# Kernel optimization log

Measured on AMD Instinct MI355X. Metric: run time of the kernel, lower is better.

The kernel has to match this reference:

```python
import jax, jax.numpy as jnp
import numpy as np

N = 50000      # nodes
E = 800000     # edges
D = 200        # in_dim = hid_dim
R = 230        # num_rels
B = 100        # bdd bases -> submat = D // B = 2
S = D // B     # submatrix size (2)


def setup_inputs() -> dict:
    key = jax.random.key(0)
    ks = jax.random.split(key, 16)
    node_feat = jax.random.normal(ks[0], (N, D), dtype=jnp.float32)
    dynamic_emb = jax.random.normal(ks[1], (N, 1, D), dtype=jnp.float32)
    src = jax.random.randint(ks[2], (E,), 0, N, dtype=jnp.int32)
    dst = jax.random.randint(ks[3], (E,), 0, N, dtype=jnp.int32)
    etypes = jax.random.randint(ks[4], (E,), 0, R, dtype=jnp.int32)
    # BDD relational weights per layer: [R, B, S, S]
    w1 = jax.random.normal(ks[5], (R, B, S, S), dtype=jnp.float32) * 0.1
    loop_w1 = jax.random.normal(ks[6], (D, D), dtype=jnp.float32) * 0.05
    b1 = jnp.zeros((D,), dtype=jnp.float32)
    w2 = jax.random.normal(ks[7], (R, B, S, S), dtype=jnp.float32) * 0.1
    loop_w2 = jax.random.normal(ks[8], (D, D), dtype=jnp.float32) * 0.05
    b2 = jnp.zeros((D,), dtype=jnp.float32)
    # single-layer vanilla RNN (tanh) params
    W_ih = jax.random.normal(ks[9], (D, D), dtype=jnp.float32) * 0.05
    W_hh = jax.random.normal(ks[10], (D, D), dtype=jnp.float32) * 0.05
    b_ih = jnp.zeros((D,), dtype=jnp.float32)
    b_hh = jnp.zeros((D,), dtype=jnp.float32)
    return {"node_feat": node_feat, "dynamic_emb": dynamic_emb,
            "src": src, "dst": dst, "etypes": etypes,
            "w1": w1, "loop_w1": loop_w1, "b1": b1,
            "w2": w2, "loop_w2": loop_w2, "b2": b2,
            "W_ih": W_ih, "W_hh": W_hh, "b_ih": b_ih, "b_hh": b_hh}


def _rel_graph_conv_bdd(x, src, dst, etypes, edge_norm, w, loop_w, b):
    # gather source feats and apply per-edge-type block-diagonal transform
    xs = x[src].reshape(E, B, S)                     # [E, B, S]
    msg = jnp.einsum('ebi,ebio->ebo', xs, w[etypes]) # [E, B, S]
    msg = msg.reshape(E, D) * edge_norm              # edge-norm scaling
    agg = jax.ops.segment_sum(msg, dst, num_segments=N)  # scatter-add to dst
    return agg + x @ loop_w + b                      # self-loop + bias


def reference(node_feat, dynamic_emb, src, dst, etypes,
              w1, loop_w1, b1, w2, loop_w2, b2,
              W_ih, W_hh, b_ih, b_hh):
    # edge_norm = dst node norm = 1 / in-degree
    deg = jax.ops.segment_sum(jnp.ones((E,), jnp.float32), dst, num_segments=N)
    node_norm = jnp.where(deg > 0, 1.0 / jnp.maximum(deg, 1.0), 0.0)
    edge_norm = node_norm[dst][:, None]              # [E, 1]

    # RGCN layer 1 (tanh activation), layer 2 (no activation); dropout=eval
    h = _rel_graph_conv_bdd(node_feat, src, dst, etypes, edge_norm, w1, loop_w1, b1)
    h = jnp.tanh(h)
    h = _rel_graph_conv_bdd(h, src, dst, etypes, edge_norm, w2, loop_w2, b2)

    # single-step vanilla RNN: hn = tanh(x W_ih^T + b_ih + h0 W_hh^T + b_hh)
    h0 = dynamic_emb[:, 0, :]                        # [N, D]
    hn = jnp.tanh(h @ W_ih.T + b_ih + h0 @ W_hh.T + b_hh)
    return hn[:, None, :]                            # [N, 1, D]
```

## Files before the change

kernel.cpp:

```cpp
#include <hip/hip_runtime.h>

#define N_NODES 50000
#define N_EDGES 800000
#define DIM     200
#define NBLK    100
#define NRELS   230
#define NB_SCAN 196
#define KPAD    224
#define KPN     256
#define NROWPAD 50048
#define NFRAG8  (8 * 14 * 64)

typedef __attribute__((ext_vector_type(8)))  short short8;
typedef __attribute__((ext_vector_type(16))) float f32x16;

__device__ __forceinline__ unsigned short f2bf(float f) {
    unsigned u = __float_as_uint(f);
    u += 0x7fffu + ((u >> 16) & 1u);
    return (unsigned short)(u >> 16);
}

__device__ __forceinline__ float bflo(unsigned u) { return __uint_as_float(u << 16); }
__device__ __forceinline__ float bfhi(unsigned u) { return __uint_as_float(u & 0xffff0000u); }
__device__ __forceinline__ float b2f(unsigned short u) { return __uint_as_float((unsigned)u << 16); }

__device__ __forceinline__ float tanh_fast(float x) {
    float xa = fminf(fmaxf(x, -15.0f), 15.0f);
    float e = __expf(2.0f * xa);
    return (e - 1.0f) / (e + 1.0f);
}

__device__ __forceinline__ int uread(int v, int l) {
    return __builtin_amdgcn_readlane(v, l);
}

#if __has_builtin(__builtin_amdgcn_fdot2_f32_bf16)
typedef __bf16 bf16x2 __attribute__((ext_vector_type(2)));
__device__ __forceinline__ float dot2bf(unsigned a, unsigned b, float c) {
    return __builtin_amdgcn_fdot2_f32_bf16(
        __builtin_bit_cast(bf16x2, a), __builtin_bit_cast(bf16x2, b), c, false);
}
#define CMP(XU, WU, M0, M1, M2, M3)                                     \
    { M0 = dot2bf(XU.x, WU.x, M0); M1 = dot2bf(XU.x, WU.y, M1);         \
      M2 = dot2bf(XU.y, WU.z, M2); M3 = dot2bf(XU.y, WU.w, M3); }
#else
#define CMP(XU, WU, M0, M1, M2, M3)                                     \
    { float x0 = bflo(XU.x), x1 = bfhi(XU.x);                           \
      float x2 = bflo(XU.y), x3 = bfhi(XU.y);                           \
      M0 += x0 * bflo(WU.x) + x1 * bfhi(WU.x);                          \
      M1 += x0 * bflo(WU.y) + x1 * bfhi(WU.y);                          \
      M2 += x2 * bflo(WU.z) + x3 * bfhi(WU.z);                          \
      M3 += x2 * bflo(WU.w) + x3 * bfhi(WU.w); }
#endif

#define SWZ5(rr, off) ((unsigned)((rr) * 512 + (off)) ^ ((unsigned)((rr) & 15) << 4))

__global__ void deg_int_kernel(const int* __restrict__ dst, int* __restrict__ degi) {
    int e = blockIdx.x * blockDim.x + threadIdx.x;
    if (e < N_EDGES) atomicAdd(&degi[dst[e]], 1);
}

__global__ __launch_bounds__(256) void scanA(const int* __restrict__ degi,
                                             int* __restrict__ pos,
                                             int* __restrict__ bsum) {
    __shared__ int tmp[256];
    int t = threadIdx.x;
    int g = blockIdx.x * 256 + t;
    int v = (g < N_NODES) ? degi[g] : 0;
    tmp[t] = v;
    __syncthreads();
    for (int off = 1; off < 256; off <<= 1) {
        int xv = (t >= off) ? tmp[t - off] : 0;
        __syncthreads();
        tmp[t] += xv;
        __syncthreads();
    }
    if (g < N_NODES) pos[g] = tmp[t] - v;
    if (t == 255) bsum[blockIdx.x] = tmp[255];
}

__global__ __launch_bounds__(256) void scanC2(int* __restrict__ pos, const int* __restrict__ bsum) {
    __shared__ int tmp[256];
    __shared__ int excl[256];
    int t = threadIdx.x;
    int v = (t < NB_SCAN) ? bsum[t] : 0;
    tmp[t] = v;
    __syncthreads();
    for (int off = 1; off < 256; off <<= 1) {
        int xv = (t >= off) ? tmp[t - off] : 0;
        __syncthreads();
        tmp[t] += xv;
        __syncthreads();
    }
    excl[t] = tmp[t] - v;
    __syncthreads();
    int add = excl[blockIdx.x];
    int g = blockIdx.x * 256 + t;
    if (g < N_NODES) pos[g] += add;
}

__global__ void fill_kernel(const int* __restrict__ src, const int* __restrict__ dst,
                            const int* __restrict__ et,
                            int* __restrict__ pos, int* __restrict__ se) {
    int e = blockIdx.x * blockDim.x + threadIdx.x;
    if (e < N_EDGES) {
        int d = dst[e];
        int slot = atomicAdd(&pos[d], 1);
        se[slot] = src[e] | (et[e] << 16);
    }
}

__global__ void prep_feat(const float* __restrict__ x, const float* __restrict__ de,
                          unsigned short* __restrict__ hb, unsigned short* __restrict__ h0b) {
    const int HALF = NROWPAD * (KPAD / 2);
    int idx = blockIdx.x * blockDim.x + threadIdx.x;
    if (idx >= 2 * HALF) return;
    const float* src = (idx < HALF) ? x : de;
    unsigned short* dstp = (idx < HALF) ? hb : h0b;
    int j = (idx < HALF) ? idx : idx - HALF;
    int row = j / (KPAD / 2), cu = j % (KPAD / 2);
    unsigned pk = 0;
    if (row < N_NODES && cu < 100) {
        float2 v = *(const float2*)(src + (size_t)row * DIM + cu * 2);
        pk = (unsigned)f2bf(v.x) | ((unsigned)f2bf(v.y) << 16);
    }
    *(unsigned*)(dstp + (size_t)j * 2) = pk;
}

__global__ void prep_wbs(const float* __restrict__ w1, const float* __restrict__ w2,
                         unsigned short* __restrict__ w1b, unsigned short* __restrict__ w2b) {
    const int HALF = NRELS * NBLK;
    int idx = blockIdx.x * blockDim.x + threadIdx.x;
    if (idx >= 2 * HALF) return;
    const float* w = (idx < HALF) ? w1 : w2;
    unsigned short* o = (idx < HALF) ? w1b : w2b;
    int j = (idx < HALF) ? idx : idx - HALF;
    float4 v = *(const float4*)(w + (size_t)j * 4);
    unsigned c0 = (unsigned)f2bf(v.x) | ((unsigned)f2bf(v.z) << 16);
    unsigned c1 = (unsigned)f2bf(v.y) | ((unsigned)f2bf(v.w) << 16);
    *(uint2*)(o + (size_t)j * 4) = make_uint2(c0, c1);
}

__global__ void prep_frags(const float* __restrict__ lw1, const float* __restrict__ wih,
                           const float* __restrict__ whh,
                           unsigned short* __restrict__ w1f, unsigned short* __restrict__ wihf,
                           unsigned short* __restrict__ whhf) {
    int idx = blockIdx.x * blockDim.x + threadIdx.x;
    if (idx >= 3 * NFRAG8) return;
    int sec = idx / NFRAG8, f = idx % NFRAG8;
    const float* w = (sec == 0) ? lw1 : (sec == 1) ? wih : whh;
    unsigned short* o = (sec == 0) ? w1f : (sec == 1) ? wihf : whhf;
    int l = f & 63;
    int ks = (f >> 6) % 14;
    int nt = f / (14 * 64);
    int n  = nt * 32 + (l & 31);
    int k0 = ks * 16 + (l >> 5) * 8;
    unsigned short v[8];
    #pragma unroll
    for (int j = 0; j < 8; ++j) {
        int k = k0 + j;
        float val = 0.0f;
        if (n < DIM && k < DIM)
            val = (sec == 0) ? w[k * DIM + n] : w[n * DIM + k];
        v[j] = f2bf(val);
    }
    *(uint4*)(o + (size_t)f * 8) = *(uint4*)v;
}

__global__ __launch_bounds__(256) void mcompute(
        const float* __restrict__ w2, const float* __restrict__ wih,
        const float* __restrict__ b2, const float* __restrict__ b_ih,
        const float* __restrict__ b_hh, float* __restrict__ Mt) {
    int idx = blockIdx.x * blockDim.x + threadIdx.x;
    if (idx >= (DIM + 1) * DIM) return;
    int k = idx / DIM, n = idx % DIM;
    const float* ar = (k < DIM) ? (w2 + (size_t)k * DIM) : b2;
    const float* br = wih + (size_t)n * DIM;
    float s0 = 0.f, s1 = 0.f, s2 = 0.f, s3 = 0.f;
    #pragma unroll 5
    for (int q = 0; q < DIM; q += 4) {
        float4 a = *(const float4*)(ar + q);
        float4 b = *(const float4*)(br + q);
        s0 += a.x * b.x; s1 += a.y * b.y; s2 += a.z * b.z; s3 += a.w * b.w;
    }
    float s = (s0 + s1) + (s2 + s3);
    if (k == DIM) s += b_ih[n] + b_hh[n];
    Mt[idx] = s;
}

__global__ void prep_Mf2(const float* __restrict__ Mt, unsigned short* __restrict__ Mf,
                         float* __restrict__ biasv) {
    int idx = blockIdx.x * blockDim.x + threadIdx.x;
    if (idx < NFRAG8) {
        int l = idx & 63;
        int ks = (idx >> 6) % 14;
        int nt = idx / (14 * 64);
        int n  = nt * 32 + (l & 31);
        int k0 = ks * 16 + (l >> 5) * 8;
        unsigned short v[8];
        #pragma unroll
        for (int j = 0; j < 8; ++j) {
            int k = k0 + j;
            v[j] = f2bf((n < DIM && k < DIM) ? Mt[k * DIM + n] : 0.0f);
        }
        *(uint4*)(Mf + (size_t)idx * 8) = *(uint4*)v;
    } else if (idx < NFRAG8 + KPN) {
        int n = idx - NFRAG8;
        biasv[n] = (n < DIM) ? Mt[DIM * DIM + n] : 0.0f;
    }
}

#define GL(QQ, XU, WU)                                                  \
    { int p_ = uread(sv, (QQ)); int s_ = p_ & 0xffff; int r_ = p_ >> 16;\
      XU = *(const uint2*)(x  + (size_t)s_ * KPAD + xoff);              \
      WU = *(const uint4*)(wb + (size_t)r_ * (NBLK * 4) + woff); }

__global__ __launch_bounds__(256) void gatherB(
        const unsigned short* __restrict__ x,
        const int*   __restrict__ se,
        const int*   __restrict__ endpos,
        const int*   __restrict__ degi,
        const unsigned short* __restrict__ wb,
        unsigned short* __restrict__ agg) {
    int node = (blockIdx.x * blockDim.x + threadIdx.x) >> 6;
    int lane = threadIdx.x & 63;
    if (node >= N_NODES) return;
    int deg = __builtin_amdgcn_readfirstlane(degi[node]);
    const bool act = (lane < 50);
    int cl   = act ? lane : 49;
    int xoff = 4 * cl;
    int woff = 8 * cl;

    if (deg == 0) {
        if (lane < 56) *(uint2*)(agg + (size_t)node * KPAD + 4 * lane) = make_uint2(0u, 0u);
        return;
    }
    int end   = __builtin_amdgcn_readfirstlane(endpos[node]);
    int start = end - deg;

    float m0A = 0.f, m1A = 0.f, m2A = 0.f, m3A = 0.f;
    float m0B = 0.f, m1B = 0.f, m2B = 0.f, m3B = 0.f;

    for (int base = start; base < end; base += 64) {
        int cnt = end - base; if (cnt > 64) cnt = 64;
        int sv = se[base + (lane < cnt ? lane : cnt - 1)];

        uint2 X0 = {0,0}, X1 = {0,0}, X2 = {0,0}, X3 = {0,0};
        uint4 W0 = {0,0,0,0}, W1 = {0,0,0,0}, W2 = {0,0,0,0}, W3 = {0,0,0,0};

        GL(0, X0, W0);
        if (cnt > 1) GL(1, X1, W1);
        if (cnt > 2) GL(2, X2, W2);

        for (int q = 0; q < cnt; q += 4) {
            if (q + 3 < cnt) GL(q + 3, X3, W3);
            CMP(X0, W0, m0A, m1A, m2A, m3A);
            if (q + 4 < cnt) GL(q + 4, X0, W0);
            if (q + 1 < cnt) CMP(X1, W1, m0B, m1B, m2B, m3B);
            if (q + 5 < cnt) GL(q + 5, X1, W1);
            if (q + 2 < cnt) CMP(X2, W2, m0A, m1A, m2A, m3A);
            if (q + 6 < cnt) GL(q + 6, X2, W2);
            if (q + 3 < cnt) CMP(X3, W3, m0B, m1B, m2B, m3B);
        }
    }
    float nrm = 1.0f / (float)deg;
    uint2 ov = make_uint2(0u, 0u);
    if (act) {
        ov.x = (unsigned)f2bf((m0A + m0B) * nrm) | ((unsigned)f2bf((m1A + m1B) * nrm) << 16);
        ov.y = (unsigned)f2bf((m2A + m2B) * nrm) | ((unsigned)f2bf((m3A + m3B) * nrm) << 16);
    }
    if (lane < 56) *(uint2*)(agg + (size_t)node * KPAD + 4 * lane) = ov;
}

__global__ __launch_bounds__(256) void gemm1_kernel(
        unsigned short* xb_hb,
        const unsigned short* __restrict__ agg1,
        const float* __restrict__ b1,
        const unsigned short* __restrict__ w1f) {
    __shared__ __align__(16) unsigned short s_a[32 * KPN];
    int row0 = blockIdx.x * 32;
    int tid = threadIdx.x;
    for (int i = tid; i < 32 * 32; i += 256) {
        int rr = i >> 5, ch = i & 31;
        uint4 v = {0, 0, 0, 0};
        if (ch < 28) v = *(const uint4*)(xb_hb + (size_t)(row0 + rr) * KPAD + ch * 8);
        *(uint4*)((char*)s_a + SWZ5(rr, ch * 16)) = v;
    }
    __syncthreads();

    int l = tid & 63, wv = tid >> 6;
    int rl = l & 31, hl = l >> 5;
    int ntlo = wv * 2;
    const unsigned short* wb = w1f + (size_t)(ntlo * 14) * 512 + l * 8;

    f32x16 acc0 = {}, acc1 = {};
    short8 aC  = *(const short8*)((const char*)s_a + SWZ5(rl, (hl * 8) * 2));
    short8 b0C = *(const short8*)(wb);
    short8 b1C = *(const short8*)(wb + 14 * 512);
    #pragma unroll
    for (int ks = 0; ks < 13; ++ks) {
        short8 aN = {}, b0N = {}, b1N = {};
        if (ks < 12) {
            aN  = *(const short8*)((const char*)s_a + SWZ5(rl, ((ks + 1) * 16 + hl * 8) * 2));
            b0N = *(const short8*)(wb + (ks + 1) * 512);
            b1N = *(const short8*)(wb + 14 * 512 + (ks + 1) * 512);
        }
        acc0 = __builtin_amdgcn_mfma_f32_32x32x16_bf16(aC, b0C, acc0, 0, 0, 0);
        acc1 = __builtin_amdgcn_mfma_f32_32x32x16_bf16(aC, b1C, acc1, 0, 0, 0);
        aC = aN; b0C = b0N; b1C = b1N;
    }
    __syncthreads();

    #pragma unroll
    for (int t = 0; t < 2; ++t) {
        f32x16 ac = t ? acc1 : acc0;
        int gc = (ntlo + t) * 32 + rl;
        if (gc >= KPAD) continue;
        float bias = (gc < DIM) ? b1[gc] : 0.0f;
        #pragma unroll
        for (int r = 0; r < 16; ++r) {
            int gr = row0 + (r & 3) + 8 * (r >> 2) + 4 * hl;
            float v = 0.0f;
            if (gc < DIM && gr < N_NODES)
                v = ac[r] + b2f(agg1[(size_t)gr * KPAD + gc]) + bias;
            xb_hb[(size_t)gr * KPAD + gc] = f2bf(tanh_fast(v));
        }
    }
}

__global__ __launch_bounds__(256) void gemm2_kernel(
        const unsigned short* __restrict__ hb,
        const unsigned short* __restrict__ aggp,
        const unsigned short* __restrict__ h0b,
        const unsigned short* __restrict__ Mf,
        const unsigned short* __restrict__ wihf,
        const unsigned short* __restrict__ whhf,
        const float* __restrict__ biasv,
        float* __restrict__ out) {
    __shared__ __align__(16) unsigned short s_h[32 * KPN];
    __shared__ __align__(16) unsigned short s_g[32 * KPN];
    __shared__ __align__(16) unsigned short s_e[32 * KPN];
    int row0 = blockIdx.x * 32;
    int tid = threadIdx.x;
    for (int i = tid; i < 32 * 32; i += 256) {
        int rr = i >> 5, ch = i & 31;
        uint4 vh = {0,0,0,0}, vg = {0,0,0,0}, ve = {0,0,0,0};
        if (ch < 28) {
            size_t off = (size_t)(row0 + rr) * KPAD + ch * 8;
            vh = *(const uint4*)(hb   + off);
            vg = *(const uint4*)(aggp + off);
            ve = *(const uint4*)(h0b  + off);
        }
        unsigned sw = SWZ5(rr, ch * 16);
        *(uint4*)((char*)s_h + sw) = vh;
        *(uint4*)((char*)s_g + sw) = vg;
        *(uint4*)((char*)s_e + sw) = ve;
    }
    __syncthreads();

    int l = tid & 63, wv = tid >> 6;
    int rl = l & 31, hl = l >> 5;
    int ntlo = wv * 2;
    const unsigned short* pm = Mf   + (size_t)(ntlo * 14) * 512 + l * 8;
    const unsigned short* pi = wihf + (size_t)(ntlo * 14) * 512 + l * 8;
    const unsigned short* ph = whhf + (size_t)(ntlo * 14) * 512 + l * 8;

    f32x16 a0 = {}, a1 = {};
    unsigned off0 = SWZ5(rl, (hl * 8) * 2);
    short8 hC  = *(const short8*)((const char*)s_h + off0);
    short8 gC  = *(const short8*)((const char*)s_g + off0);
    short8 eC  = *(const short8*)((const char*)s_e + off0);
    short8 m0C = *(const short8*)(pm);
    short8 m1C = *(const short8*)(pm + 14 * 512);
    short8 i0C = *(const short8*)(pi);
    short8 i1C = *(const short8*)(pi + 14 * 512);
    short8 h0C = *(const short8*)(ph);
    short8 h1C = *(const short8*)(ph + 14 * 512);
    #pragma unroll
    for (int ks = 0; ks < 13; ++ks) {
        short8 hN = {}, gN = {}, eN = {};
        short8 m0N = {}, m1N = {}, i0N = {}, i1N = {}, h0N = {}, h1N = {};
        if (ks < 12) {
            unsigned off = SWZ5(rl, ((ks + 1) * 16 + hl * 8) * 2);
            hN  = *(const short8*)((const char*)s_h + off);
            gN  = *(const short8*)((const char*)s_g + off);
            eN  = *(const short8*)((const char*)s_e + off);
            m0N = *(const short8*)(pm + (ks + 1) * 512);
            m1N = *(const short8*)(pm + 14 * 512 + (ks + 1) * 512);
            i0N = *(const short8*)(pi + (ks + 1) * 512);
            i1N = *(const short8*)(pi + 14 * 512 + (ks + 1) * 512);
            h0N = *(const short8*)(ph + (ks + 1) * 512);
            h1N = *(const short8*)(ph + 14 * 512 + (ks + 1) * 512);
        }
        a0 = __builtin_amdgcn_mfma_f32_32x32x16_bf16(hC, m0C, a0, 0, 0, 0);
        a0 = __builtin_amdgcn_mfma_f32_32x32x16_bf16(gC, i0C, a0, 0, 0, 0);
        a0 = __builtin_amdgcn_mfma_f32_32x32x16_bf16(eC, h0C, a0, 0, 0, 0);
        a1 = __builtin_amdgcn_mfma_f32_32x32x16_bf16(hC, m1C, a1, 0, 0, 0);
        a1 = __builtin_amdgcn_mfma_f32_32x32x16_bf16(gC, i1C, a1, 0, 0, 0);
        a1 = __builtin_amdgcn_mfma_f32_32x32x16_bf16(eC, h1C, a1, 0, 0, 0);
        hC = hN; gC = gN; eC = eN;
        m0C = m0N; m1C = m1N; i0C = i0N; i1C = i1N; h0C = h0N; h1C = h1N;
    }

    #pragma unroll
    for (int t = 0; t < 2; ++t) {
        f32x16 oc = t ? a1 : a0;
        int gc = (ntlo + t) * 32 + rl;
        if (gc >= DIM) continue;
        float bias = biasv[gc];
        #pragma unroll
        for (int r = 0; r < 16; ++r) {
            int gr = row0 + (r & 3) + 8 * (r >> 2) + 4 * hl;
            if (gr < N_NODES)
                out[(size_t)gr * DIM + gc] = tanh_fast(oc[r] + bias);
        }
    }
}

extern "C" void kernel_launch(void* const* d_in, const int* in_sizes, int n_in,
                              void* d_out, int out_size, void* d_ws, size_t ws_size,
                              hipStream_t stream) {
    const float* node_feat = (const float*)d_in[0];
    const float* dyn_emb   = (const float*)d_in[1];
    const int*   src       = (const int*)  d_in[2];
    const int*   dst       = (const int*)  d_in[3];
    const int*   etypes    = (const int*)  d_in[4];
    const float* w1        = (const float*)d_in[5];
    const float* loop_w1   = (const float*)d_in[6];
    const float* b1        = (const float*)d_in[7];
    const float* w2        = (const float*)d_in[8];
    const float* loop_w2   = (const float*)d_in[9];
    const float* b2        = (const float*)d_in[10];
    const float* W_ih      = (const float*)d_in[11];
    const float* W_hh      = (const float*)d_in[12];
    const float* b_ih      = (const float*)d_in[13];
    const float* b_hh      = (const float*)d_in[14];
    float* out = (float*)d_out;

    int*   degi = (int*)d_ws;
    int*   pos  = degi + 51200;
    int*   bsum = pos  + 51200;
    int*   se   = bsum + 256;
    unsigned short* aggp = (unsigned short*)(se + N_EDGES);
    unsigned short* hb   = aggp + (size_t)NROWPAD * KPAD;
    unsigned short* h0b  = hb   + (size_t)NROWPAD * KPAD;
    unsigned short* w1f  = h0b  + (size_t)NROWPAD * KPAD;
    unsigned short* wihf = w1f  + (size_t)NFRAG8 * 8;
    unsigned short* whhf = wihf + (size_t)NFRAG8 * 8;
    unsigned short* Mf   = whhf + (size_t)NFRAG8 * 8;
    unsigned short* w1b  = Mf   + (size_t)NFRAG8 * 8;
    unsigned short* w2b  = w1b  + (size_t)NRELS * NBLK * 4;
    float* biasv = (float*)(w2b + (size_t)NRELS * NBLK * 4);
    float* Mt    = biasv + KPN;

    hipMemsetAsync(degi, 0, 51200 * sizeof(int), stream);

    deg_int_kernel<<<(N_EDGES + 255) / 256, 256, 0, stream>>>(dst, degi);
    scanA<<<NB_SCAN, 256, 0, stream>>>(degi, pos, bsum);
    scanC2<<<NB_SCAN, 256, 0, stream>>>(pos, bsum);
    fill_kernel<<<(N_EDGES + 255) / 256, 256, 0, stream>>>(src, dst, etypes, pos, se);

    prep_feat<<<(2 * NROWPAD * (KPAD / 2) + 255) / 256, 256, 0, stream>>>(
        node_feat, dyn_emb, hb, h0b);
    prep_wbs<<<(2 * NRELS * NBLK + 255) / 256, 256, 0, stream>>>(w1, w2, w1b, w2b);
    prep_frags<<<(3 * NFRAG8 + 255) / 256, 256, 0, stream>>>(
        loop_w1, W_ih, W_hh, w1f, wihf, whhf);
    mcompute<<<((DIM + 1) * DIM + 255) / 256, 256, 0, stream>>>(
        loop_w2, W_ih, b2, b_ih, b_hh, Mt);
    prep_Mf2<<<(NFRAG8 + KPN + 255) / 256, 256, 0, stream>>>(Mt, Mf, biasv);

    gatherB<<<(N_NODES * 64 + 255) / 256, 256, 0, stream>>>(
        hb, se, pos, degi, w1b, aggp);
    gemm1_kernel<<<(N_NODES + 31) / 32, 256, 0, stream>>>(
        hb, aggp, b1, w1f);

    gatherB<<<(N_NODES * 64 + 255) / 256, 256, 0, stream>>>(
        hb, se, pos, degi, w2b, aggp);

    gemm2_kernel<<<(N_NODES + 31) / 32, 256, 0, stream>>>(
        hb, aggp, h0b, Mf, wihf, whhf, biasv, out);
}
```

Measured before the change: 338.6 us.

## Fuse preprocessing kernels, pad CSR rows to multiples of four, convert h0 inline

Folds degree counting, feature and weight conversion, and M precompute into one launch, and CSR fill, padding and Mf packing into a second, removing several kernel launches. Each node's edge list is padded to a multiple of four using a dummy zero row, so the gather loop drops its per-edge bounds checks and runs a simpler 8-deep prefetch with one accumulator set. gemm2 now reads dynamic_emb in fp32 and converts to bf16 in shared memory, which removes the separate h0 bf16 buffer and its write pass. The costs are extra padded gathers from the dummy row and a serial dependency chain on a single set of accumulators in the gather.

```diff
diff --git a/kernel.cpp b/kernel.cpp
--- a/kernel.cpp
+++ b/kernel.cpp
@@ -10,6 +10,8 @@
 #define KPN     256
 #define NROWPAD 50048
 #define NFRAG8  (8 * 14 * 64)
+#define EPADMAX (N_EDGES + 3 * N_NODES + 16)
+#define DUMMYROW 50000
 
 typedef __attribute__((ext_vector_type(8)))  short short8;
 typedef __attribute__((ext_vector_type(16))) float f32x16;
@@ -40,33 +42,116 @@
     return __builtin_amdgcn_fdot2_f32_bf16(
         __builtin_bit_cast(bf16x2, a), __builtin_bit_cast(bf16x2, b), c, false);
 }
-#define CMP(XU, WU, M0, M1, M2, M3)                                     \
-    { M0 = dot2bf(XU.x, WU.x, M0); M1 = dot2bf(XU.x, WU.y, M1);         \
-      M2 = dot2bf(XU.y, WU.z, M2); M3 = dot2bf(XU.y, WU.w, M3); }
+#define CMP4(XU, WU)                                                    \
+    { m0 = dot2bf(XU.x, WU.x, m0); m1 = dot2bf(XU.x, WU.y, m1);         \
+      m2 = dot2bf(XU.y, WU.z, m2); m3 = dot2bf(XU.y, WU.w, m3); }
 #else
-#define CMP(XU, WU, M0, M1, M2, M3)                                     \
+#define CMP4(XU, WU)                                                    \
     { float x0 = bflo(XU.x), x1 = bfhi(XU.x);                           \
       float x2 = bflo(XU.y), x3 = bfhi(XU.y);                           \
-      M0 += x0 * bflo(WU.x) + x1 * bfhi(WU.x);                          \
-      M1 += x0 * bflo(WU.y) + x1 * bfhi(WU.y);                          \
-      M2 += x2 * bflo(WU.z) + x3 * bfhi(WU.z);                          \
-      M3 += x2 * bflo(WU.w) + x3 * bfhi(WU.w); }
+      m0 += x0 * bflo(WU.x) + x1 * bfhi(WU.x);                          \
+      m1 += x0 * bflo(WU.y) + x1 * bfhi(WU.y);                          \
+      m2 += x2 * bflo(WU.z) + x3 * bfhi(WU.z);                          \
+      m3 += x2 * bflo(WU.w) + x3 * bfhi(WU.w); }
 #endif
 
 #define SWZ5(rr, off) ((unsigned)((rr) * 512 + (off)) ^ ((unsigned)((rr) & 15) << 4))
 
-__global__ void deg_int_kernel(const int* __restrict__ dst, int* __restrict__ degi) {
-    int e = blockIdx.x * blockDim.x + threadIdx.x;
-    if (e < N_EDGES) atomicAdd(&degi[dst[e]], 1);
+#define M1_A N_EDGES
+#define M1_B (NROWPAD * (KPAD / 2))
+#define M1_C (2 * NRELS * NBLK)
+#define M1_D (3 * NFRAG8)
+#define M1_E ((DIM + 1) * DIM)
+#define M1_TOTAL (M1_A + M1_B + M1_C + M1_D + M1_E)
+
+__global__ __launch_bounds__(256) void mega1(
+        const int* __restrict__ dst, int* __restrict__ degi,
+        const float* __restrict__ node_feat, unsigned short* __restrict__ xb,
+        const float* __restrict__ w1, const float* __restrict__ w2,
+        unsigned short* __restrict__ w1b, unsigned short* __restrict__ w2b,
+        const float* __restrict__ lw1, const float* __restrict__ wih,
+        const float* __restrict__ whh,
+        unsigned short* __restrict__ w1f, unsigned short* __restrict__ wihf,
+        unsigned short* __restrict__ whhf,
+        const float* __restrict__ lw2, const float* __restrict__ b2,
+        const float* __restrict__ b_ih, const float* __restrict__ b_hh,
+        float* __restrict__ Mt) {
+    int idx = blockIdx.x * blockDim.x + threadIdx.x;
+    if (idx < M1_A) {
+        atomicAdd(&degi[dst[idx]], 1);
+        return;
+    }
+    idx -= M1_A;
+    if (idx < M1_B) {
+        int row = idx / (KPAD / 2), cu = idx % (KPAD / 2);
+        unsigned pk = 0;
+        if (row < N_NODES && cu < 100) {
+            float2 v = *(const float2*)(node_feat + (size_t)row * DIM + cu * 2);
+            pk = (unsigned)f2bf(v.x) | ((unsigned)f2bf(v.y) << 16);
+        }
+        *(unsigned*)(xb + (size_t)idx * 2) = pk;
+        return;
+    }
+    idx -= M1_B;
+    if (idx < M1_C) {
+        const int HALF = NRELS * NBLK;
+        const float* w = (idx < HALF) ? w1 : w2;
+        unsigned short* o = (idx < HALF) ? w1b : w2b;
+        int j = (idx < HALF) ? idx : idx - HALF;
+        float4 v = *(const float4*)(w + (size_t)j * 4);
+        unsigned c0 = (unsigned)f2bf(v.x) | ((unsigned)f2bf(v.z) << 16);
+        unsigned c1 = (unsigned)f2bf(v.y) | ((unsigned)f2bf(v.w) << 16);
+        *(uint2*)(o + (size_t)j * 4) = make_uint2(c0, c1);
+        return;
+    }
+    idx -= M1_C;
+    if (idx < M1_D) {
+        int sec = idx / NFRAG8, f = idx % NFRAG8;
+        const float* w = (sec == 0) ? lw1 : (sec == 1) ? wih : whh;
+        unsigned short* o = (sec == 0) ? w1f : (sec == 1) ? wihf : whhf;
+        int l = f & 63;
+        int ks = (f >> 6) % 14;
+        int nt = f / (14 * 64);
+        int n  = nt * 32 + (l & 31);
+        int k0 = ks * 16 + (l >> 5) * 8;
+        unsigned short v[8];
+        #pragma unroll
+        for (int j = 0; j < 8; ++j) {
+            int k = k0 + j;
+            float val = 0.0f;
+            if (n < DIM && k < DIM)
+                val = (sec == 0) ? w[k * DIM + n] : w[n * DIM + k];
+            v[j] = f2bf(val);
+        }
+        *(uint4*)(o + (size_t)f * 8) = *(uint4*)v;
+        return;
+    }
+    idx -= M1_D;
+    if (idx < M1_E) {
+        int k = idx / DIM, n = idx % DIM;
+        const float* ar = (k < DIM) ? (lw2 + (size_t)k * DIM) : b2;
+        const float* br = wih + (size_t)n * DIM;
+        float s0 = 0.f, s1 = 0.f, s2 = 0.f, s3 = 0.f;
+        #pragma unroll 5
+        for (int q = 0; q < DIM; q += 4) {
+            float4 a = *(const float4*)(ar + q);
+            float4 b = *(const float4*)(br + q);
+            s0 += a.x * b.x; s1 += a.y * b.y; s2 += a.z * b.z; s3 += a.w * b.w;
+        }
+        float s = (s0 + s1) + (s2 + s3);
+        if (k == DIM) s += b_ih[n] + b_hh[n];
+        Mt[idx] = s;
+    }
 }
 
 __global__ __launch_bounds__(256) void scanA(const int* __restrict__ degi,
-                                             int* __restrict__ pos,
+                                             int* __restrict__ pos, int* __restrict__ cur,
                                              int* __restrict__ bsum) {
     __shared__ int tmp[256];
     int t = threadIdx.x;
     int g = blockIdx.x * 256 + t;
-    int v = (g < N_NODES) ? degi[g] : 0;
+    int d = (g < N_NODES) ? degi[g] : 0;
+    int v = (d + 3) & ~3;
     tmp[t] = v;
     __syncthreads();
     for (int off = 1; off < 256; off <<= 1) {
@@ -75,11 +160,12 @@
         tmp[t] += xv;
         __syncthreads();
     }
-    if (g < N_NODES) pos[g] = tmp[t] - v;
+    if (g < N_NODES) { int e = tmp[t] - v; pos[g] = e; cur[g] = e; }
     if (t == 255) bsum[blockIdx.x] = tmp[255];
 }
 
-__global__ __launch_bounds__(256) void scanC2(int* __restrict__ pos, const int* __restrict__ bsum) {
+__global__ __launch_bounds__(256) void scanC2(int* __restrict__ pos, int* __restrict__ cur,
+                                              const int* __restrict__ bsum) {
     __shared__ int tmp[256];
     __shared__ int excl[256];
     int t = threadIdx.x;
@@ -96,101 +182,39 @@
     __syncthreads();
     int add = excl[blockIdx.x];
     int g = blockIdx.x * 256 + t;
-    if (g < N_NODES) pos[g] += add;
-}
-
-__global__ void fill_kernel(const int* __restrict__ src, const int* __restrict__ dst,
-                            const int* __restrict__ et,
-                            int* __restrict__ pos, int* __restrict__ se) {
-    int e = blockIdx.x * blockDim.x + threadIdx.x;
-    if (e < N_EDGES) {
-        int d = dst[e];
-        int slot = atomicAdd(&pos[d], 1);
-        se[slot] = src[e] | (et[e] << 16);
-    }
-}
-
-__global__ void prep_feat(const float* __restrict__ x, const float* __restrict__ de,
-                          unsigned short* __restrict__ hb, unsigned short* __restrict__ h0b) {
-    const int HALF = NROWPAD * (KPAD / 2);
+    if (g < N_NODES) { pos[g] += add; cur[g] += add; }
+}
+
+#define M2_A N_EDGES
+#define M2_B N_NODES
+#define M2_C (NFRAG8 + KPN)
+#define M2_TOTAL (M2_A + M2_B + M2_C)
+
+__global__ __launch_bounds__(256) void mega2(
+        const int* __restrict__ src, const int* __restrict__ dst,
+        const int* __restrict__ et,
+        int* __restrict__ cur, const int* __restrict__ pos,
+        const int* __restrict__ degi, int* __restrict__ se,
+        const float* __restrict__ Mt, unsigned short* __restrict__ Mf,
+        float* __restrict__ biasv) {
     int idx = blockIdx.x * blockDim.x + threadIdx.x;
-    if (idx >= 2 * HALF) return;
-    const float* src = (idx < HALF) ? x : de;
-    unsigned short* dstp = (idx < HALF) ? hb : h0b;
-    int j = (idx < HALF) ? idx : idx - HALF;
-    int row = j / (KPAD / 2), cu = j % (KPAD / 2);
-    unsigned pk = 0;
-    if (row < N_NODES && cu < 100) {
-        float2 v = *(const float2*)(src + (size_t)row * DIM + cu * 2);
-        pk = (unsigned)f2bf(v.x) | ((unsigned)f2bf(v.y) << 16);
-    }
-    *(unsigned*)(dstp + (size_t)j * 2) = pk;
-}
-
-__global__ void prep_wbs(const float* __restrict__ w1, const float* __restrict__ w2,
-                         unsigned short* __restrict__ w1b, unsigned short* __restrict__ w2b) {
-    const int HALF = NRELS * NBLK;
-    int idx = blockIdx.x * blockDim.x + threadIdx.x;
-    if (idx >= 2 * HALF) return;
-    const float* w = (idx < HALF) ? w1 : w2;
-    unsigned short* o = (idx < HALF) ? w1b : w2b;
-    int j = (idx < HALF) ? idx : idx - HALF;
-    float4 v = *(const float4*)(w + (size_t)j * 4);
-    unsigned c0 = (unsigned)f2bf(v.x) | ((unsigned)f2bf(v.z) << 16);
-    unsigned c1 = (unsigned)f2bf(v.y) | ((unsigned)f2bf(v.w) << 16);
-    *(uint2*)(o + (size_t)j * 4) = make_uint2(c0, c1);
-}
-
-__global__ void prep_frags(const float* __restrict__ lw1, const float* __restrict__ wih,
-                           const float* __restrict__ whh,
-                           unsigned short* __restrict__ w1f, unsigned short* __restrict__ wihf,
-                           unsigned short* __restrict__ whhf) {
-    int idx = blockIdx.x * blockDim.x + threadIdx.x;
-    if (idx >= 3 * NFRAG8) return;
-    int sec = idx / NFRAG8, f = idx % NFRAG8;
-    const float* w = (sec == 0) ? lw1 : (sec == 1) ? wih : whh;
-    unsigned short* o = (sec == 0) ? w1f : (sec == 1) ? wihf : whhf;
-    int l = f & 63;
-    int ks = (f >> 6) % 14;
-    int nt = f / (14 * 64);
-    int n  = nt * 32 + (l & 31);
-    int k0 = ks * 16 + (l >> 5) * 8;
-    unsigned short v[8];
-    #pragma unroll
-    for (int j = 0; j < 8; ++j) {
-        int k = k0 + j;
-        float val = 0.0f;
-        if (n < DIM && k < DIM)
-            val = (sec == 0) ? w[k * DIM + n] : w[n * DIM + k];
-        v[j] = f2bf(val);
-    }
-    *(uint4*)(o + (size_t)f * 8) = *(uint4*)v;
-}
-
-__global__ __launch_bounds__(256) void mcompute(
-        const float* __restrict__ w2, const float* __restrict__ wih,
-        const float* __restrict__ b2, const float* __restrict__ b_ih,
-        const float* __restrict__ b_hh, float* __restrict__ Mt) {
-    int idx = blockIdx.x * blockDim.x + threadIdx.x;
-    if (idx >= (DIM + 1) * DIM) return;
-    int k = idx / DIM, n = idx % DIM;
-    const float* ar = (k < DIM) ? (w2 + (size_t)k * DIM) : b2;
-    const float* br = wih + (size_t)n * DIM;
-    float s0 = 0.f, s1 = 0.f, s2 = 0.f, s3 = 0.f;
-    #pragma unroll 5
-    for (int q = 0; q < DIM; q += 4) {
-        float4 a = *(const float4*)(ar + q);
-        float4 b = *(const float4*)(br + q);
-        s0 += a.x * b.x; s1 += a.y * b.y; s2 += a.z * b.z; s3 += a.w * b.w;
-    }
-    float s = (s0 + s1) + (s2 + s3);
-    if (k == DIM) s += b_ih[n] + b_hh[n];
-    Mt[idx] = s;
-}
-
-__global__ void prep_Mf2(const float* __restrict__ Mt, unsigned short* __restrict__ Mf,
-                         float* __restrict__ biasv) {
-    int idx = blockIdx.x * blockDim.x + threadIdx.x;
+    if (idx < M2_A) {
+        int d = dst[idx];
+        int slot = atomicAdd(&cur[d], 1);
+        se[slot] = src[idx] | (et[idx] << 16);
+        return;
+    }
+    idx -= M2_A;
+    if (idx < M2_B) {
+        int d = degi[idx];
+        if (d > 0) {
+            int dp = (d + 3) & ~3;
+            int start = pos[idx];
+            for (int j = d; j < dp; ++j) se[start + j] = DUMMYROW;
+        }
+        return;
+    }
+    idx -= M2_B;
     if (idx < NFRAG8) {
         int l = idx & 63;
         int ks = (idx >> 6) % 14;
@@ -218,7 +242,7 @@
 __global__ __launch_bounds__(256) void gatherB(
         const unsigned short* __restrict__ x,
         const int*   __restrict__ se,
-        const int*   __restrict__ endpos,
+        const int*   __restrict__ pstart,
         const int*   __restrict__ degi,
         const unsigned short* __restrict__ wb,
         unsigned short* __restrict__ agg) {
@@ -235,39 +259,34 @@
         if (lane < 56) *(uint2*)(agg + (size_t)node * KPAD + 4 * lane) = make_uint2(0u, 0u);
         return;
     }
-    int end   = __builtin_amdgcn_readfirstlane(endpos[node]);
-    int start = end - deg;
-
-    float m0A = 0.f, m1A = 0.f, m2A = 0.f, m3A = 0.f;
-    float m0B = 0.f, m1B = 0.f, m2B = 0.f, m3B = 0.f;
-
-    for (int base = start; base < end; base += 64) {
-        int cnt = end - base; if (cnt > 64) cnt = 64;
-        int sv = se[base + (lane < cnt ? lane : cnt - 1)];
-
-        uint2 X0 = {0,0}, X1 = {0,0}, X2 = {0,0}, X3 = {0,0};
-        uint4 W0 = {0,0,0,0}, W1 = {0,0,0,0}, W2 = {0,0,0,0}, W3 = {0,0,0,0};
-
-        GL(0, X0, W0);
-        if (cnt > 1) GL(1, X1, W1);
-        if (cnt > 2) GL(2, X2, W2);
-
-        for (int q = 0; q < cnt; q += 4) {
-            if (q + 3 < cnt) GL(q + 3, X3, W3);
-            CMP(X0, W0, m0A, m1A, m2A, m3A);
-            if (q + 4 < cnt) GL(q + 4, X0, W0);
-            if (q + 1 < cnt) CMP(X1, W1, m0B, m1B, m2B, m3B);
-            if (q + 5 < cnt) GL(q + 5, X1, W1);
-            if (q + 2 < cnt) CMP(X2, W2, m0A, m1A, m2A, m3A);
-            if (q + 6 < cnt) GL(q + 6, X2, W2);
-            if (q + 3 < cnt) CMP(X3, W3, m0B, m1B, m2B, m3B);
+    int start = __builtin_amdgcn_readfirstlane(pstart[node]);
+    int degp  = (deg + 3) & ~3;
+
+    float m0 = 0.f, m1 = 0.f, m2 = 0.f, m3 = 0.f;
+
+    for (int base = 0; base < degp; base += 64) {
+        int cnt = degp - base; if (cnt > 64) cnt = 64;
+        int sv = se[start + base + (lane < cnt ? lane : cnt - 1)];
+
+        uint2 X0, X1, X2, X3, Y0, Y1, Y2, Y3;
+        uint4 W0, W1, W2, W3, V0, V1, V2, V3;
+        GL(0, X0, W0); GL(1, X1, W1); GL(2, X2, W2); GL(3, X3, W3);
+
+        for (int q = 0; q < cnt; q += 8) {
+            bool l1 = (q + 4 < cnt);
+            if (l1) { GL(q + 4, Y0, V0); GL(q + 5, Y1, V1); GL(q + 6, Y2, V2); GL(q + 7, Y3, V3); }
+            CMP4(X0, W0); CMP4(X1, W1); CMP4(X2, W2); CMP4(X3, W3);
+            if (!l1) break;
+            bool l2 = (q + 8 < cnt);
+            if (l2) { GL(q + 8, X0, W0); GL(q + 9, X1, W1); GL(q + 10, X2, W2); GL(q + 11, X3, W3); }
+            CMP4(Y0, V0); CMP4(Y1, V1); CMP4(Y2, V2); CMP4(Y3, V3);
         }
     }
     float nrm = 1.0f / (float)deg;
     uint2 ov = make_uint2(0u, 0u);
     if (act) {
-        ov.x = (unsigned)f2bf((m0A + m0B) * nrm) | ((unsigned)f2bf((m1A + m1B) * nrm) << 16);
-        ov.y = (unsigned)f2bf((m2A + m2B) * nrm) | ((unsigned)f2bf((m3A + m3B) * nrm) << 16);
+        ov.x = (unsigned)f2bf(m0 * nrm) | ((unsigned)f2bf(m1 * nrm) << 16);
+        ov.y = (unsigned)f2bf(m2 * nrm) | ((unsigned)f2bf(m3 * nrm) << 16);
     }
     if (lane < 56) *(uint2*)(agg + (size_t)node * KPAD + 4 * lane) = ov;
 }
@@ -331,7 +350,7 @@
 __global__ __launch_bounds__(256) void gemm2_kernel(
         const unsigned short* __restrict__ hb,
         const unsigned short* __restrict__ aggp,
-        const unsigned short* __restrict__ h0b,
+        const float* __restrict__ h0,
         const unsigned short* __restrict__ Mf,
         const unsigned short* __restrict__ wihf,
         const unsigned short* __restrict__ whhf,
@@ -344,17 +363,25 @@
     int tid = threadIdx.x;
     for (int i = tid; i < 32 * 32; i += 256) {
         int rr = i >> 5, ch = i & 31;
-        uint4 vh = {0,0,0,0}, vg = {0,0,0,0}, ve = {0,0,0,0};
+        uint4 vh = {0,0,0,0}, vg = {0,0,0,0};
         if (ch < 28) {
             size_t off = (size_t)(row0 + rr) * KPAD + ch * 8;
             vh = *(const uint4*)(hb   + off);
             vg = *(const uint4*)(aggp + off);
-            ve = *(const uint4*)(h0b  + off);
         }
         unsigned sw = SWZ5(rr, ch * 16);
         *(uint4*)((char*)s_h + sw) = vh;
         *(uint4*)((char*)s_g + sw) = vg;
-        *(uint4*)((char*)s_e + sw) = ve;
+    }
+    for (int i = tid; i < 32 * 128; i += 256) {
+        int rr = i >> 7, cu = i & 127;
+        int gr = row0 + rr;
+        unsigned pk = 0;
+        if (cu < 100 && gr < N_NODES) {
+            float2 v = *(const float2*)(h0 + (size_t)gr * DIM + cu * 2);
+            pk = (unsigned)f2bf(v.x) | ((unsigned)f2bf(v.y) << 16);
+        }
+        *(unsigned*)((char*)s_e + SWZ5(rr, cu * 4)) = pk;
     }
     __syncthreads();
 
@@ -393,10 +420,10 @@
             h1N = *(const short8*)(ph + 14 * 512 + (ks + 1) * 512);
         }
         a0 = __builtin_amdgcn_mfma_f32_32x32x16_bf16(hC, m0C, a0, 0, 0, 0);
+        a1 = __builtin_amdgcn_mfma_f32_32x32x16_bf16(hC, m1C, a1, 0, 0, 0);
         a0 = __builtin_amdgcn_mfma_f32_32x32x16_bf16(gC, i0C, a0, 0, 0, 0);
+        a1 = __builtin_amdgcn_mfma_f32_32x32x16_bf16(gC, i1C, a1, 0, 0, 0);
         a0 = __builtin_amdgcn_mfma_f32_32x32x16_bf16(eC, h0C, a0, 0, 0, 0);
-        a1 = __builtin_amdgcn_mfma_f32_32x32x16_bf16(hC, m1C, a1, 0, 0, 0);
-        a1 = __builtin_amdgcn_mfma_f32_32x32x16_bf16(gC, i1C, a1, 0, 0, 0);
         a1 = __builtin_amdgcn_mfma_f32_32x32x16_bf16(eC, h1C, a1, 0, 0, 0);
         hC = hN; gC = gN; eC = eN;
         m0C = m0N; m1C = m1N; i0C = i0N; i1C = i1N; h0C = h0N; h1C = h1N;
@@ -439,12 +466,12 @@
 
     int*   degi = (int*)d_ws;
     int*   pos  = degi + 51200;
-    int*   bsum = pos  + 51200;
+    int*   cur  = pos  + 51200;
+    int*   bsum = cur  + 51200;
     int*   se   = bsum + 256;
-    unsigned short* aggp = (unsigned short*)(se + N_EDGES);
+    unsigned short* aggp = (unsigned short*)(se + EPADMAX);
     unsigned short* hb   = aggp + (size_t)NROWPAD * KPAD;
-    unsigned short* h0b  = hb   + (size_t)NROWPAD * KPAD;
-    unsigned short* w1f  = h0b  + (size_t)NROWPAD * KPAD;
+    unsigned short* w1f  = hb   + (size_t)NROWPAD * KPAD;
     unsigned short* wihf = w1f  + (size_t)NFRAG8 * 8;
     unsigned short* whhf = wihf + (size_t)NFRAG8 * 8;
     unsigned short* Mf   = whhf + (size_t)NFRAG8 * 8;
@@ -455,19 +482,16 @@
 
     hipMemsetAsync(degi, 0, 51200 * sizeof(int), stream);
 
-    deg_int_kernel<<<(N_EDGES + 255) / 256, 256, 0, stream>>>(dst, degi);
-    scanA<<<NB_SCAN, 256, 0, stream>>>(degi, pos, bsum);
-    scanC2<<<NB_SCAN, 256, 0, stream>>>(pos, bsum);
-    fill_kernel<<<(N_EDGES + 255) / 256, 256, 0, stream>>>(src, dst, etypes, pos, se);
-
-    prep_feat<<<(2 * NROWPAD * (KPAD / 2) + 255) / 256, 256, 0, stream>>>(
-        node_feat, dyn_emb, hb, h0b);
-    prep_wbs<<<(2 * NRELS * NBLK + 255) / 256, 256, 0, stream>>>(w1, w2, w1b, w2b);
-    prep_frags<<<(3 * NFRAG8 + 255) / 256, 256, 0, stream>>>(
-        loop_w1, W_ih, W_hh, w1f, wihf, whhf);
-    mcompute<<<((DIM + 1) * DIM + 255) / 256, 256, 0, stream>>>(
-        loop_w2, W_ih, b2, b_ih, b_hh, Mt);
-    prep_Mf2<<<(NFRAG8 + KPN + 255) / 256, 256, 0, stream>>>(Mt, Mf, biasv);
+    mega1<<<(M1_TOTAL + 255) / 256, 256, 0, stream>>>(
+        dst, degi, node_feat, hb, w1, w2, w1b, w2b,
+        loop_w1, W_ih, W_hh, w1f, wihf, whhf,
+        loop_w2, b2, b_ih, b_hh, Mt);
+
+    scanA<<<NB_SCAN, 256, 0, stream>>>(degi, pos, cur, bsum);
+    scanC2<<<NB_SCAN, 256, 0, stream>>>(pos, cur, bsum);
+
+    mega2<<<(M2_TOTAL + 255) / 256, 256, 0, stream>>>(
+        src, dst, etypes, cur, pos, degi, se, Mt, Mf, biasv);
 
     gatherB<<<(N_NODES * 64 + 255) / 256, 256, 0, stream>>>(
         hb, se, pos, degi, w1b, aggp);
@@ -478,5 +502,5 @@
         hb, se, pos, degi, w2b, aggp);
 
     gemm2_kernel<<<(N_NODES + 31) / 32, 256, 0, stream>>>(
-        hb, aggp, h0b, Mf, wihf, whhf, biasv, out);
-}
+        hb, aggp, dyn_emb, Mf, wihf, whhf, biasv, out);
+}
```

Result: slower. 364.3 us (+7.6%).
